# Performance work log

Hardware: AMD Instinct MI355X
Metric: run time of the kernel (lower is better)

The kernel has to match this reference:

```python
import jax, jax.numpy as jnp
import numpy as np
import math

D_MODEL = 1024
N_HEADS = 16
HEAD_DIM = D_MODEL // N_HEADS  # 64
R = HEAD_DIM // 2              # 32
ROPE_BASE = 10000.0
B, T = 4, 2048


def setup_inputs() -> dict:
    key = jax.random.key(0)
    k1, k2, k3, k4, k5 = jax.random.split(key, 5)
    x = jax.random.normal(k1, (B, T, D_MODEL), dtype=jnp.float32)
    Wqkv = jax.random.normal(k2, (3 * D_MODEL, D_MODEL), dtype=jnp.float32) * (1.0 / math.sqrt(D_MODEL))
    Wout = jax.random.normal(k3, (D_MODEL, D_MODEL), dtype=jnp.float32) * (1.0 / math.sqrt(D_MODEL))
    alpha = jax.random.normal(k4, (N_HEADS, R), dtype=jnp.float32) * 0.01
    beta = jax.random.normal(k5, (N_HEADS, R), dtype=jnp.float32) * 0.01
    return {"x": x, "Wqkv": Wqkv, "Wout": Wout, "alpha": alpha, "beta": beta}


def _fourier_bias(alpha, beta, t):
    # omega[r] = base^{-2r/head_dim}, same geometric spacing as RoPE
    omega = ROPE_BASE ** (-2.0 * jnp.arange(R, dtype=jnp.float32) / HEAD_DIM)
    # bias depends only on displacement i-j in [-(t-1), t-1]: compute once per
    # displacement, then gather into the (t, t) matrix (same math as full T x T).
    disp = jnp.arange(-(t - 1), t, dtype=jnp.float32)            # (2t-1,)
    angles = omega[:, None] * disp[None, :]                       # (R, 2t-1)
    vec = jnp.einsum('hr,rk->hk', alpha, jnp.cos(angles)) \
        + jnp.einsum('hr,rk->hk', beta, jnp.sin(angles))          # (H, 2t-1)
    i = jnp.arange(t)
    idx = i[:, None] - i[None, :] + (t - 1)                       # (t, t), delta[i,j]=i-j
    return vec[:, idx]                                            # (H, t, t)


def reference(x, Wqkv, Wout, alpha, beta):
    b, t, d = x.shape
    qkv = x @ Wqkv.T                                              # (B, T, 3D)
    q, k, v = jnp.split(qkv, 3, axis=-1)
    def heads(a):
        return a.reshape(b, t, N_HEADS, HEAD_DIM).transpose(0, 2, 1, 3)  # (B,H,T,dh)
    q, k, v = heads(q), heads(k), heads(v)
    scale = 1.0 / math.sqrt(HEAD_DIM)
    logits = jnp.einsum('bhqd,bhkd->bhqk', q, k) * scale          # (B,H,T,T)
    logits = logits + _fourier_bias(alpha, beta, t)[None]
    causal = jnp.tril(jnp.ones((t, t), dtype=bool))
    logits = jnp.where(causal[None, None], logits, -jnp.inf)
    attn = jax.nn.softmax(logits, axis=-1)
    out = jnp.einsum('bhqk,bhkd->bhqd', attn, v)                  # (B,H,T,dh)
    out = out.transpose(0, 2, 1, 3).reshape(b, t, d)
    return out @ Wout.T
```

## Files before the change

### kernel.cpp

```cpp
#include <hip/hip_runtime.h>
#include <cstdint>
#include <cstddef>

typedef _Float16 f16;
typedef f16 f16x8 __attribute__((ext_vector_type(8)));
typedef __fp16 fp16x2 __attribute__((ext_vector_type(2)));
typedef float f32x4 __attribute__((ext_vector_type(4)));
typedef float f32x16 __attribute__((ext_vector_type(16)));
typedef uint32_t u32;


__device__ __forceinline__ void gload16(const void* g, void* l) {
  __builtin_amdgcn_global_load_lds((const __attribute__((address_space(1))) void*)g,
                                   (__attribute__((address_space(3))) void*)l,
                                   16u, 0, 0u);
}

__device__ __forceinline__ u32 pkrtz(float a, float b) {
  union { fp16x2 v; u32 u; } t;
  t.v = __builtin_amdgcn_cvt_pkrtz(a, b);
  return t.u;
}

__device__ __forceinline__ u32 packh2(float a, float b) { return pkrtz(a, b); }

__device__ __forceinline__ float max3f(float a, float b, float c) {
  return fmaxf(fmaxf(a, b), c);
}

__device__ __forceinline__ void pl32swap(u32& a, u32& b) {
  asm volatile("v_permlane32_swap_b32 %0, %1" : "+v"(a), "+v"(b));
}


__global__ __launch_bounds__(256) void cvt_f32_f16(const float* __restrict__ in,
                                                   f16* __restrict__ out, int n) {
  int i = (blockIdx.x * 256 + threadIdx.x) * 8;
  if (i >= n) return;
  float4 a = *(const float4*)(in + i);
  float4 b = *(const float4*)(in + i + 4);
  f16x8 o;
  o[0] = (f16)a.x; o[1] = (f16)a.y; o[2] = (f16)a.z; o[3] = (f16)a.w;
  o[4] = (f16)b.x; o[5] = (f16)b.y; o[6] = (f16)b.z; o[7] = (f16)b.w;
  *(f16x8*)(out + i) = o;
}


__global__ __launch_bounds__(256) void build_tables(const float* __restrict__ alpha,
                                                    const float* __restrict__ beta,
                                                    f16* __restrict__ U,
                                                    f16* __restrict__ Wt) {
  int idx = blockIdx.x * 256 + threadIdx.x;
  int t = idx >> 5, r = idx & 31;
  float w = powf(10000.0f, -(float)r / 32.0f);
  float ang = w * (float)t;
  float c = cosf(ang), s = sinf(ang);
  const float L2E = 1.44269504089f;
  U[t * 64 + 2 * r]     = (f16)(c * L2E);
  U[t * 64 + 2 * r + 1] = (f16)(s * L2E);
  #pragma unroll
  for (int h = 0; h < 16; ++h) {
    float al = alpha[h * 32 + r], be = beta[h * 32 + r];
    Wt[(size_t)(h * 2048 + t) * 64 + 2 * r]     = (f16)(al * c - be * s);
    Wt[(size_t)(h * 2048 + t) * 64 + 2 * r + 1] = (f16)(al * s + be * c);
  }
}



__global__ __launch_bounds__(512, 2) void gemm_qkv(const f16* __restrict__ A,
                                                   const f16* __restrict__ B,
                                                   f16* __restrict__ Q,
                                                   f16* __restrict__ Kh,
                                                   f16* __restrict__ Vt) {
  __shared__ __align__(16) char sm[147456];
  const int K = 1024;
  int tid = threadIdx.x;
  int lane = tid & 63, wid = tid >> 6;
  int bid = blockIdx.x;
  int xcd = bid & 7;
  int id = bid >> 3;
  int ml = id / 24;
  int nn = id % 24;
  int m0 = (xcd * 4 + ml) * 256;
  int n0 = nn * 128;
  int wm = wid >> 1, wn = wid & 1;
  int c = lane & 15, g = lane >> 4;
  int swz = (c & 7) << 4;

  const f16* asrc[4]; int adst[4];
  #pragma unroll
  for (int i = 0; i < 4; ++i) {
    int p = i * 8192 + tid * 16;
    int row = p >> 7;
    int col = (p & 127) ^ ((row & 7) << 4);
    asrc[i] = A + (size_t)(m0 + row) * K + (col >> 1);
    adst[i] = i * 8192 + wid * 1024;
  }
  const f16* bsrc[2]; int bdst[2];
  #pragma unroll
  for (int i = 0; i < 2; ++i) {
    int p = i * 8192 + tid * 16;
    int row = p >> 7;
    int col = (p & 127) ^ ((row & 7) << 4);
    bsrc[i] = B + (size_t)(n0 + row) * K + (col >> 1);
    bdst[i] = i * 8192 + wid * 1024;
  }

  f32x4 acc[4][4] = {};

  #pragma unroll
  for (int i = 0; i < 4; ++i) gload16(asrc[i], sm + adst[i]);
  #pragma unroll
  for (int i = 0; i < 2; ++i) gload16(bsrc[i], sm + 98304 + bdst[i]);
  #pragma unroll
  for (int i = 0; i < 4; ++i) gload16(asrc[i] + 64, sm + 32768 + adst[i]);
  #pragma unroll
  for (int i = 0; i < 2; ++i) gload16(bsrc[i] + 64, sm + 98304 + 16384 + bdst[i]);

  for (int kt = 0; kt < 16; ++kt) {
    if (kt < 15) asm volatile("s_waitcnt vmcnt(6)" ::: "memory");
    else         asm volatile("s_waitcnt vmcnt(0)" ::: "memory");
    __builtin_amdgcn_s_barrier();

    int j = kt % 3;
    char* As = sm + j * 32768;
    char* Bs = sm + 98304 + j * 16384;
    int jn = (kt + 2) % 3;
    char* Ad = sm + jn * 32768;
    char* Bd = sm + 98304 + jn * 16384;
    bool stg = (kt <= 13);

    if (stg) {
      gload16(asrc[0] + (kt + 2) * 64, Ad + adst[0]);
      gload16(asrc[1] + (kt + 2) * 64, Ad + adst[1]);
      gload16(asrc[2] + (kt + 2) * 64, Ad + adst[2]);
    }
    {
      int co = (g * 16) ^ swz;
      f16x8 af[4], bf[4];
      #pragma unroll
      for (int fr = 0; fr < 4; ++fr)
        af[fr] = *(const f16x8*)(As + (wm * 64 + fr * 16 + c) * 128 + co);
      #pragma unroll
      for (int fn = 0; fn < 4; ++fn)
        bf[fn] = *(const f16x8*)(Bs + (wn * 64 + fn * 16 + c) * 128 + co);
      __builtin_amdgcn_s_setprio(1);
      #pragma unroll
      for (int fr = 0; fr < 4; ++fr)
        #pragma unroll
        for (int fn = 0; fn < 4; ++fn)
          acc[fr][fn] = __builtin_amdgcn_mfma_f32_16x16x32_f16(af[fr], bf[fn], acc[fr][fn], 0, 0, 0);
      __builtin_amdgcn_s_setprio(0);
    }
    if (stg) {
      gload16(asrc[3] + (kt + 2) * 64, Ad + adst[3]);
      gload16(bsrc[0] + (kt + 2) * 64, Bd + bdst[0]);
      gload16(bsrc[1] + (kt + 2) * 64, Bd + bdst[1]);
    }
    {
      int co = (64 + g * 16) ^ swz;
      f16x8 af[4], bf[4];
      #pragma unroll
      for (int fr = 0; fr < 4; ++fr)
        af[fr] = *(const f16x8*)(As + (wm * 64 + fr * 16 + c) * 128 + co);
      #pragma unroll
      for (int fn = 0; fn < 4; ++fn)
        bf[fn] = *(const f16x8*)(Bs + (wn * 64 + fn * 16 + c) * 128 + co);
      __builtin_amdgcn_s_setprio(1);
      #pragma unroll
      for (int fr = 0; fr < 4; ++fr)
        #pragma unroll
        for (int fn = 0; fn < 4; ++fn)
          acc[fr][fn] = __builtin_amdgcn_mfma_f32_16x16x32_f16(af[fr], bf[fn], acc[fr][fn], 0, 0, 0);
      __builtin_amdgcn_s_setprio(0);
    }
  }

  int which = n0 >> 10;
  #pragma unroll
  for (int fr = 0; fr < 4; ++fr) {
    int m = m0 + wm * 64 + fr * 16 + g * 4;
    int b = m >> 11, t = m & 2047;
    #pragma unroll
    for (int fn = 0; fn < 4; ++fn) {
      int n = n0 + wn * 64 + fn * 16 + c;
      int nf = n & 1023, hh = nf >> 6, d = nf & 63;
      if (which == 0) {
        #pragma unroll
        for (int r = 0; r < 4; ++r)
          Q[(size_t)((b * 16 + hh) * 2048 + (t + r)) * 64 + d] = (f16)(acc[fr][fn][r] * 0.180336880111f);
      } else if (which == 1) {
        #pragma unroll
        for (int r = 0; r < 4; ++r)
          Kh[(size_t)((b * 16 + hh) * 2048 + (t + r)) * 64 + d] = (f16)acc[fr][fn][r];
      } else {
        uint2 pk;
        pk.x = packh2(acc[fr][fn][0], acc[fr][fn][1]);
        pk.y = packh2(acc[fr][fn][2], acc[fr][fn][3]);
        *(uint2*)(Vt + (size_t)((b * 16 + hh) * 64 + d) * 2048 + t) = pk;
      }
    }
  }
}


__global__ __launch_bounds__(512, 2) void gemm_out(const f16* __restrict__ A,
                                                   const f16* __restrict__ B,
                                                   float* __restrict__ Cout) {
  __shared__ __align__(16) char sm[147456];
  const int K = 1024;
  int tid = threadIdx.x;
  int lane = tid & 63, wid = tid >> 6;
  int bid = blockIdx.x;
  int xcd = bid & 7;
  int id = bid >> 3;
  int m0 = (xcd * 4 + id / 8) * 256;
  int n0 = (id & 7) * 128;
  int wm = wid >> 1, wn = wid & 1;
  int c = lane & 15, g = lane >> 4;
  int swz = (c & 7) << 4;

  const f16* asrc[4]; int adst[4];
  #pragma unroll
  for (int i = 0; i < 4; ++i) {
    int p = i * 8192 + tid * 16;
    int row = p >> 7;
    int col = (p & 127) ^ ((row & 7) << 4);
    asrc[i] = A + (size_t)(m0 + row) * K + (col >> 1);
    adst[i] = i * 8192 + wid * 1024;
  }
  const f16* bsrc[2]; int bdst[2];
  #pragma unroll
  for (int i = 0; i < 2; ++i) {
    int p = i * 8192 + tid * 16;
    int row = p >> 7;
    int col = (p & 127) ^ ((row & 7) << 4);
    bsrc[i] = B + (size_t)(n0 + row) * K + (col >> 1);
    bdst[i] = i * 8192 + wid * 1024;
  }

  f32x4 acc[4][4] = {};

  #pragma unroll
  for (int i = 0; i < 4; ++i) gload16(asrc[i], sm + adst[i]);
  #pragma unroll
  for (int i = 0; i < 2; ++i) gload16(bsrc[i], sm + 98304 + bdst[i]);
  #pragma unroll
  for (int i = 0; i < 4; ++i) gload16(asrc[i] + 64, sm + 32768 + adst[i]);
  #pragma unroll
  for (int i = 0; i < 2; ++i) gload16(bsrc[i] + 64, sm + 98304 + 16384 + bdst[i]);

  for (int kt = 0; kt < 16; ++kt) {
    if (kt < 15) asm volatile("s_waitcnt vmcnt(6)" ::: "memory");
    else         asm volatile("s_waitcnt vmcnt(0)" ::: "memory");
    __builtin_amdgcn_s_barrier();

    int j = kt % 3;
    char* As = sm + j * 32768;
    char* Bs = sm + 98304 + j * 16384;
    int jn = (kt + 2) % 3;
    char* Ad = sm + jn * 32768;
    char* Bd = sm + 98304 + jn * 16384;
    bool stg = (kt <= 13);

    if (stg) {
      gload16(asrc[0] + (kt + 2) * 64, Ad + adst[0]);
      gload16(asrc[1] + (kt + 2) * 64, Ad + adst[1]);
      gload16(asrc[2] + (kt + 2) * 64, Ad + adst[2]);
    }
    {
      int co = (g * 16) ^ swz;
      f16x8 af[4], bf[4];
      #pragma unroll
      for (int fr = 0; fr < 4; ++fr)
        af[fr] = *(const f16x8*)(As + (wm * 64 + fr * 16 + c) * 128 + co);
      #pragma unroll
      for (int fn = 0; fn < 4; ++fn)
        bf[fn] = *(const f16x8*)(Bs + (wn * 64 + fn * 16 + c) * 128 + co);
      __builtin_amdgcn_s_setprio(1);
      #pragma unroll
      for (int fr = 0; fr < 4; ++fr)
        #pragma unroll
        for (int fn = 0; fn < 4; ++fn)
          acc[fr][fn] = __builtin_amdgcn_mfma_f32_16x16x32_f16(af[fr], bf[fn], acc[fr][fn], 0, 0, 0);
      __builtin_amdgcn_s_setprio(0);
    }
    if (stg) {
      gload16(asrc[3] + (kt + 2) * 64, Ad + adst[3]);
      gload16(bsrc[0] + (kt + 2) * 64, Bd + bdst[0]);
      gload16(bsrc[1] + (kt + 2) * 64, Bd + bdst[1]);
    }
    {
      int co = (64 + g * 16) ^ swz;
      f16x8 af[4], bf[4];
      #pragma unroll
      for (int fr = 0; fr < 4; ++fr)
        af[fr] = *(const f16x8*)(As + (wm * 64 + fr * 16 + c) * 128 + co);
      #pragma unroll
      for (int fn = 0; fn < 4; ++fn)
        bf[fn] = *(const f16x8*)(Bs + (wn * 64 + fn * 16 + c) * 128 + co);
      __builtin_amdgcn_s_setprio(1);
      #pragma unroll
      for (int fr = 0; fr < 4; ++fr)
        #pragma unroll
        for (int fn = 0; fn < 4; ++fn)
          acc[fr][fn] = __builtin_amdgcn_mfma_f32_16x16x32_f16(af[fr], bf[fn], acc[fr][fn], 0, 0, 0);
      __builtin_amdgcn_s_setprio(0);
    }
  }

  #pragma unroll
  for (int fr = 0; fr < 4; ++fr) {
    int m = m0 + wm * 64 + fr * 16 + g * 4;
    #pragma unroll
    for (int fn = 0; fn < 4; ++fn) {
      int n = n0 + wn * 64 + fn * 16 + c;
      #pragma unroll
      for (int r = 0; r < 4; ++r)
        Cout[(size_t)(m + r) * 1024 + n] = acc[fr][fn][r];
    }
  }
}


__global__ __launch_bounds__(512, 2) void attn(const f16* __restrict__ Q,
                                               const f16* __restrict__ Kh,
                                               const f16* __restrict__ Vt,
                                               const f16* __restrict__ U,
                                               const f16* __restrict__ Wt,
                                               f16* __restrict__ AO) {
  __shared__ __align__(16) char sm[98304];
  int tid = threadIdx.x, lane = tid & 63, wid = tid >> 6;
  int l31 = lane & 31, hi = lane >> 5;
  int o = blockIdx.x;
  int pr = o >> 6;
  int bh = o & 63;
  int h = bh & 15, b = bh >> 4;
  int swz = (lane & 15) << 4;

  const f16* ksrc[4]; int kdst[4];
  #pragma unroll
  for (int i = 0; i < 4; ++i) {
    int p = i * 8192 + tid * 16;
    int row = p >> 8;
    int col = (p & 255) ^ ((row & 15) << 4);
    int ce = col >> 1;
    ksrc[i] = (ce < 64) ? (Kh + (size_t)(bh * 2048 + row) * 64 + ce)
                        : (Wt + (size_t)(h * 2048 + row) * 64 + (ce - 64));
    kdst[i] = i * 8192 + wid * 1024;
  }
  const f16* vsrc[2]; int vdst[2];
  #pragma unroll
  for (int i = 0; i < 2; ++i) {
    int p = i * 8192 + tid * 16;
    int row = p >> 8;
    int col = (p & 255) ^ ((row & 15) << 4);
    int ce = col >> 1;
    vsrc[i] = Vt + (size_t)(bh * 64 + row) * 2048 + ce;
    vdst[i] = i * 8192 + wid * 1024;
  }

  #pragma unroll 1
  for (int pass = 0; pass < 2; ++pass) {
    int qt = pass ? pr : 7 - pr;
    int qrow = qt * 256 + wid * 32 + l31;
    int ktmax = 2 * qt + 1;

    f16x8 qf[8];
    {
      const f16* qp = Q + (size_t)(bh * 2048 + qrow) * 64 + hi * 8;
      const f16* up = U + (size_t)qrow * 64 + hi * 8;
      #pragma unroll
      for (int ks = 0; ks < 4; ++ks) {
        qf[ks]     = *(const f16x8*)(qp + ks * 16);
        qf[4 + ks] = *(const f16x8*)(up + ks * 16);
      }
    }

    float m_i = -1e30f, l_i = 0.0f;
    f32x16 accA = {}, accB = {};

    #pragma unroll
    for (int i = 0; i < 4; ++i) gload16(ksrc[i], sm + kdst[i]);
    #pragma unroll
    for (int i = 0; i < 2; ++i) gload16(vsrc[i], sm + 65536 + vdst[i]);
    __syncthreads();

    for (int kt = 0; kt <= ktmax; ++kt) {
      int cur = kt & 1;
      char* Ks = sm + cur * 32768;
      char* Vs = sm + 65536 + cur * 16384;

      if (kt < ktmax) {
        char* kb = sm + (cur ^ 1) * 32768;
        char* vb = sm + 65536 + (cur ^ 1) * 16384;
        #pragma unroll
        for (int i = 0; i < 4; ++i) gload16(ksrc[i] + (size_t)(kt + 1) * 8192, kb + kdst[i]);
        #pragma unroll
        for (int i = 0; i < 2; ++i) gload16(vsrc[i] + (size_t)(kt + 1) * 128, vb + vdst[i]);
      }

      f32x16 st0 = {}, st1 = {}, st2 = {}, st3 = {};
      __builtin_amdgcn_s_setprio(1);
      #pragma unroll
      for (int ks = 0; ks < 8; ++ks) {
        int co = (ks * 32 + hi * 16) ^ swz;
        f16x8 k0 = *(const f16x8*)(Ks + l31 * 256 + co);
        f16x8 k1 = *(const f16x8*)(Ks + (32 + l31) * 256 + co);
        f16x8 k2 = *(const f16x8*)(Ks + (64 + l31) * 256 + co);
        f16x8 k3 = *(const f16x8*)(Ks + (96 + l31) * 256 + co);
        st0 = __builtin_amdgcn_mfma_f32_32x32x16_f16(k0, qf[ks], st0, 0, 0, 0);
        st1 = __builtin_amdgcn_mfma_f32_32x32x16_f16(k1, qf[ks], st1, 0, 0, 0);
        st2 = __builtin_amdgcn_mfma_f32_32x32x16_f16(k2, qf[ks], st2, 0, 0, 0);
        st3 = __builtin_amdgcn_mfma_f32_32x32x16_f16(k3, qf[ks], st3, 0, 0, 0);
      }
      __builtin_amdgcn_s_setprio(0);

      int kv0 = kt * 128;
      if (kv0 + 127 > qt * 256 + wid * 32) {
        #pragma unroll
        for (int r = 0; r < 16; ++r) {
          int kvl = kv0 + (r & 3) + 8 * (r >> 2) + 4 * hi;
          if (kvl > qrow) st0[r] = -1e30f;
          if (kvl + 32 > qrow) st1[r] = -1e30f;
          if (kvl + 64 > qrow) st2[r] = -1e30f;
          if (kvl + 96 > qrow) st3[r] = -1e30f;
        }
      }

      float pm = fmaxf(fmaxf(st0[0], st1[0]), fmaxf(st2[0], st3[0]));
      #pragma unroll
      for (int r = 1; r < 16; ++r) {
        pm = max3f(pm, st0[r], st1[r]);
        pm = max3f(pm, st2[r], st3[r]);
      }
      pm = fmaxf(pm, __shfl_xor(pm, 32, 64));
      if (!__all(pm <= m_i + 8.0f)) {
        float mnew = fmaxf(m_i, pm);
        float sc = __builtin_amdgcn_exp2f(m_i - mnew);
        l_i *= sc;
        accA *= sc;
        accB *= sc;
        m_i = mnew;
      }

      float ps = 0.0f;
      u32 pk0[8], pk1[8], pk2[8], pk3[8];
      #pragma unroll
      for (int j = 0; j < 8; ++j) {
        float a0 = __builtin_amdgcn_exp2f(st0[2 * j] - m_i);
        float a1 = __builtin_amdgcn_exp2f(st0[2 * j + 1] - m_i);
        float b0 = __builtin_amdgcn_exp2f(st1[2 * j] - m_i);
        float b1 = __builtin_amdgcn_exp2f(st1[2 * j + 1] - m_i);
        float c0 = __builtin_amdgcn_exp2f(st2[2 * j] - m_i);
        float c1 = __builtin_amdgcn_exp2f(st2[2 * j + 1] - m_i);
        float d0 = __builtin_amdgcn_exp2f(st3[2 * j] - m_i);
        float d1 = __builtin_amdgcn_exp2f(st3[2 * j + 1] - m_i);
        ps += (a0 + a1) + (b0 + b1) + (c0 + c1) + (d0 + d1);
        pk0[j] = pkrtz(a0, a1);
        pk1[j] = pkrtz(b0, b1);
        pk2[j] = pkrtz(c0, c1);
        pk3[j] = pkrtz(d0, d1);
      }
      ps += __shfl_xor(ps, 32, 64);
      l_i += ps;

      pl32swap(pk0[0], pk0[2]); pl32swap(pk0[1], pk0[3]);
      pl32swap(pk0[4], pk0[6]); pl32swap(pk0[5], pk0[7]);
      pl32swap(pk1[0], pk1[2]); pl32swap(pk1[1], pk1[3]);
      pl32swap(pk1[4], pk1[6]); pl32swap(pk1[5], pk1[7]);
      pl32swap(pk2[0], pk2[2]); pl32swap(pk2[1], pk2[3]);
      pl32swap(pk2[4], pk2[6]); pl32swap(pk2[5], pk2[7]);
      pl32swap(pk3[0], pk3[2]); pl32swap(pk3[1], pk3[3]);
      pl32swap(pk3[4], pk3[6]); pl32swap(pk3[5], pk3[7]);

      __builtin_amdgcn_s_setprio(1);
      #pragma unroll
      for (int kb = 0; kb < 8; ++kb) {
        union { u32 w[4]; f16x8 v; } bf;
        const u32* pk = (kb < 2) ? pk0 : (kb < 4) ? pk1 : (kb < 6) ? pk2 : pk3;
        int base = (kb & 1) * 4;
        bf.w[0] = pk[base + 0]; bf.w[1] = pk[base + 1];
        bf.w[2] = pk[base + 2]; bf.w[3] = pk[base + 3];
        int co = (kb * 32 + hi * 16) ^ swz;
        f16x8 v0 = *(const f16x8*)(Vs + l31 * 256 + co);
        f16x8 v1 = *(const f16x8*)(Vs + (32 + l31) * 256 + co);
        accA = __builtin_amdgcn_mfma_f32_32x32x16_f16(v0, bf.v, accA, 0, 0, 0);
        accB = __builtin_amdgcn_mfma_f32_32x32x16_f16(v1, bf.v, accB, 0, 0, 0);
      }
      __builtin_amdgcn_s_setprio(0);
      __syncthreads();
    }

    float inv = __builtin_amdgcn_rcpf(l_i);
    f16* aop = AO + (size_t)(b * 2048 + qrow) * 1024 + h * 64;
    #pragma unroll
    for (int u = 0; u < 4; ++u) {
      uint2 ov;
      ov.x = pkrtz(accA[4 * u] * inv, accA[4 * u + 1] * inv);
      ov.y = pkrtz(accA[4 * u + 2] * inv, accA[4 * u + 3] * inv);
      *(uint2*)(aop + 8 * u + 4 * hi) = ov;
      ov.x = pkrtz(accB[4 * u] * inv, accB[4 * u + 1] * inv);
      ov.y = pkrtz(accB[4 * u + 2] * inv, accB[4 * u + 3] * inv);
      *(uint2*)(aop + 32 + 8 * u + 4 * hi) = ov;
    }
  }
}


extern "C" void kernel_launch(void* const* d_in, const int* in_sizes, int n_in,
                              void* d_out, int out_size, void* d_ws, size_t ws_size,
                              hipStream_t stream) {
  const float* x     = (const float*)d_in[0];
  const float* Wqkv  = (const float*)d_in[1];
  const float* Wout  = (const float*)d_in[2];
  const float* alpha = (const float*)d_in[3];
  const float* beta  = (const float*)d_in[4];

  char* ws = (char*)d_ws;
  f16* Xh    = (f16*)(ws);
  f16* Wqkvh = (f16*)(ws + 16777216);
  f16* Wouth = (f16*)(ws + 23068672);
  f16* Qh    = (f16*)(ws + 25165824);
  f16* Kh    = (f16*)(ws + 41943040);
  f16* Vt    = (f16*)(ws + 58720256);
  f16* U     = (f16*)(ws + 75497472);
  f16* Wt    = (f16*)(ws + 75759616);
  f16* AO    = Xh;

  cvt_f32_f16<<<4096, 256, 0, stream>>>(x, Xh, 8388608);
  cvt_f32_f16<<<1536, 256, 0, stream>>>(Wqkv, Wqkvh, 3145728);
  cvt_f32_f16<<<512, 256, 0, stream>>>(Wout, Wouth, 1048576);
  build_tables<<<256, 256, 0, stream>>>(alpha, beta, U, Wt);
  gemm_qkv<<<768, 512, 0, stream>>>(Xh, Wqkvh, Qh, Kh, Vt);
  attn<<<256, 512, 0, stream>>>(Qh, Kh, Vt, U, Wt, AO);
  gemm_out<<<256, 512, 0, stream>>>(AO, Wouth, (float*)d_out);
}
```

Measured before the change: 165.1 us.

## Apply Fourier bias as multiplicative exp factor instead of extra QK dimensions

```diff
diff --git a/kernel.cpp b/kernel.cpp
--- a/kernel.cpp
+++ b/kernel.cpp
@@ -23,6 +23,13 @@
 }
 
 __device__ __forceinline__ u32 packh2(float a, float b) { return pkrtz(a, b); }
+
+__device__ __forceinline__ u32 pkmul(u32 a, u32 b) {
+  union { fp16x2 v; u32 u; } x, y, r;
+  x.u = a; y.u = b;
+  r.v = x.v * y.v;
+  return r.u;
+}
 
 __device__ __forceinline__ float max3f(float a, float b, float c) {
   return fmaxf(fmaxf(a, b), c);
@@ -46,26 +53,41 @@
 }
 
 
-__global__ __launch_bounds__(256) void build_tables(const float* __restrict__ alpha,
-                                                    const float* __restrict__ beta,
-                                                    f16* __restrict__ U,
-                                                    f16* __restrict__ Wt) {
+__global__ __launch_bounds__(256) void build_bias(const float* __restrict__ alpha,
+                                                  const float* __restrict__ beta,
+                                                  float* __restrict__ Bias) {
+  int d = blockIdx.x * 256 + threadIdx.x;
+  if (d >= 4095) return;
+  float delta = (float)(d - 2047);
+  float acc[16];
+  #pragma unroll
+  for (int h = 0; h < 16; ++h) acc[h] = 0.0f;
+  for (int r = 0; r < 32; ++r) {
+    float w = powf(10000.0f, -(float)r / 32.0f);
+    float ang = w * delta;
+    float c = cosf(ang), s = sinf(ang);
+    #pragma unroll
+    for (int h = 0; h < 16; ++h)
+      acc[h] += alpha[h * 32 + r] * c + beta[h * 32 + r] * s;
+  }
+  #pragma unroll
+  for (int h = 0; h < 16; ++h) Bias[h * 4095 + d] = acc[h];
+}
+
+__global__ __launch_bounds__(256) void pack_F(const float* __restrict__ Bias,
+                                              uint2* __restrict__ Fdup) {
   int idx = blockIdx.x * 256 + threadIdx.x;
-  int t = idx >> 5, r = idx & 31;
-  float w = powf(10000.0f, -(float)r / 32.0f);
-  float ang = w * (float)t;
-  float c = cosf(ang), s = sinf(ang);
-  const float L2E = 1.44269504089f;
-  U[t * 64 + 2 * r]     = (f16)(c * L2E);
-  U[t * 64 + 2 * r + 1] = (f16)(s * L2E);
-  #pragma unroll
-  for (int h = 0; h < 16; ++h) {
-    float al = alpha[h * 32 + r], be = beta[h * 32 + r];
-    Wt[(size_t)(h * 2048 + t) * 64 + 2 * r]     = (f16)(al * c - be * s);
-    Wt[(size_t)(h * 2048 + t) * 64 + 2 * r + 1] = (f16)(al * s + be * c);
-  }
-}
-
+  if (idx >= 16 * 4095) return;
+  int h = idx / 4095, d = idx - h * 4095;
+  const float* Bh = Bias + h * 4095;
+  int d1 = d - 1 < 0 ? 0 : d - 1;
+  int d2 = d - 2 < 0 ? 0 : d - 2;
+  int d3 = d - 3 < 0 ? 0 : d - 3;
+  uint2 o;
+  o.x = pkrtz(expf(Bh[d]),  expf(Bh[d1]));
+  o.y = pkrtz(expf(Bh[d2]), expf(Bh[d3]));
+  Fdup[idx] = o;
+}
 
 
 __global__ __launch_bounds__(512, 2) void gemm_qkv(const f16* __restrict__ A,
@@ -327,27 +349,27 @@
 __global__ __launch_bounds__(512, 2) void attn(const f16* __restrict__ Q,
                                                const f16* __restrict__ Kh,
                                                const f16* __restrict__ Vt,
-                                               const f16* __restrict__ U,
-                                               const f16* __restrict__ Wt,
+                                               const uint2* __restrict__ Fdup,
                                                f16* __restrict__ AO) {
-  __shared__ __align__(16) char sm[98304];
+  __shared__ __align__(16) char sm[65536];
   int tid = threadIdx.x, lane = tid & 63, wid = tid >> 6;
   int l31 = lane & 31, hi = lane >> 5;
   int o = blockIdx.x;
   int pr = o >> 6;
   int bh = o & 63;
   int h = bh & 15, b = bh >> 4;
-  int swz = (lane & 15) << 4;
-
-  const f16* ksrc[4]; int kdst[4];
-  #pragma unroll
-  for (int i = 0; i < 4; ++i) {
+  int swzK = (lane & 7) << 4;
+  int swzV = (lane & 15) << 4;
+
+  const uint2* Fp = Fdup + (size_t)h * 4095;
+
+  const f16* ksrc[2]; int kdst[2];
+  #pragma unroll
+  for (int i = 0; i < 2; ++i) {
     int p = i * 8192 + tid * 16;
-    int row = p >> 8;
-    int col = (p & 255) ^ ((row & 15) << 4);
-    int ce = col >> 1;
-    ksrc[i] = (ce < 64) ? (Kh + (size_t)(bh * 2048 + row) * 64 + ce)
-                        : (Wt + (size_t)(h * 2048 + row) * 64 + (ce - 64));
+    int row = p >> 7;
+    int col = (p & 127) ^ ((row & 7) << 4);
+    ksrc[i] = Kh + (size_t)(bh * 2048 + row) * 64 + (col >> 1);
     kdst[i] = i * 8192 + wid * 1024;
   }
   const f16* vsrc[2]; int vdst[2];
@@ -356,8 +378,7 @@
     int p = i * 8192 + tid * 16;
     int row = p >> 8;
     int col = (p & 255) ^ ((row & 15) << 4);
-    int ce = col >> 1;
-    vsrc[i] = Vt + (size_t)(bh * 64 + row) * 2048 + ce;
+    vsrc[i] = Vt + (size_t)(bh * 64 + row) * 2048 + (col >> 1);
     vdst[i] = i * 8192 + wid * 1024;
   }
 
@@ -367,49 +388,55 @@
     int qrow = qt * 256 + wid * 32 + l31;
     int ktmax = 2 * qt + 1;
 
-    f16x8 qf[8];
+    f16x8 qf[4];
     {
       const f16* qp = Q + (size_t)(bh * 2048 + qrow) * 64 + hi * 8;
-      const f16* up = U + (size_t)qrow * 64 + hi * 8;
-      #pragma unroll
-      for (int ks = 0; ks < 4; ++ks) {
-        qf[ks]     = *(const f16x8*)(qp + ks * 16);
-        qf[4 + ks] = *(const f16x8*)(up + ks * 16);
-      }
+      #pragma unroll
+      for (int ks = 0; ks < 4; ++ks) qf[ks] = *(const f16x8*)(qp + ks * 16);
     }
 
     float m_i = -1e30f, l_i = 0.0f;
     f32x16 accA = {}, accB = {};
 
     #pragma unroll
-    for (int i = 0; i < 4; ++i) gload16(ksrc[i], sm + kdst[i]);
+    for (int i = 0; i < 2; ++i) gload16(ksrc[i], sm + kdst[i]);
     #pragma unroll
-    for (int i = 0; i < 2; ++i) gload16(vsrc[i], sm + 65536 + vdst[i]);
+    for (int i = 0; i < 2; ++i) gload16(vsrc[i], sm + 32768 + vdst[i]);
     __syncthreads();
 
     for (int kt = 0; kt <= ktmax; ++kt) {
       int cur = kt & 1;
-      char* Ks = sm + cur * 32768;
-      char* Vs = sm + 65536 + cur * 16384;
+      char* Ks = sm + cur * 16384;
+      char* Vs = sm + 32768 + cur * 16384;
 
       if (kt < ktmax) {
-        char* kb = sm + (cur ^ 1) * 32768;
-        char* vb = sm + 65536 + (cur ^ 1) * 16384;
-        #pragma unroll
-        for (int i = 0; i < 4; ++i) gload16(ksrc[i] + (size_t)(kt + 1) * 8192, kb + kdst[i]);
+        char* kb = sm + (cur ^ 1) * 16384;
+        char* vb = sm + 32768 + (cur ^ 1) * 16384;
+        #pragma unroll
+        for (int i = 0; i < 2; ++i) gload16(ksrc[i] + (size_t)(kt + 1) * 8192, kb + kdst[i]);
         #pragma unroll
         for (int i = 0; i < 2; ++i) gload16(vsrc[i] + (size_t)(kt + 1) * 128, vb + vdst[i]);
+      }
+
+      int fidx = qrow - kt * 128 - 4 * hi + 2047;
+      uint2 fw0[4], fw1[4], fw2[4], fw3[4];
+      #pragma unroll
+      for (int rg = 0; rg < 4; ++rg) {
+        fw0[rg] = Fp[fidx - rg * 8];
+        fw1[rg] = Fp[fidx - 32 - rg * 8];
+        fw2[rg] = Fp[fidx - 64 - rg * 8];
+        fw3[rg] = Fp[fidx - 96 - rg * 8];
       }
 
       f32x16 st0 = {}, st1 = {}, st2 = {}, st3 = {};
       __builtin_amdgcn_s_setprio(1);
       #pragma unroll
-      for (int ks = 0; ks < 8; ++ks) {
-        int co = (ks * 32 + hi * 16) ^ swz;
-        f16x8 k0 = *(const f16x8*)(Ks + l31 * 256 + co);
-        f16x8 k1 = *(const f16x8*)(Ks + (32 + l31) * 256 + co);
-        f16x8 k2 = *(const f16x8*)(Ks + (64 + l31) * 256 + co);
-        f16x8 k3 = *(const f16x8*)(Ks + (96 + l31) * 256 + co);
+      for (int ks = 0; ks < 4; ++ks) {
+        int co = (ks * 32 + hi * 16) ^ swzK;
+        f16x8 k0 = *(const f16x8*)(Ks + l31 * 128 + co);
+        f16x8 k1 = *(const f16x8*)(Ks + (32 + l31) * 128 + co);
+        f16x8 k2 = *(const f16x8*)(Ks + (64 + l31) * 128 + co);
+        f16x8 k3 = *(const f16x8*)(Ks + (96 + l31) * 128 + co);
         st0 = __builtin_amdgcn_mfma_f32_32x32x16_f16(k0, qf[ks], st0, 0, 0, 0);
         st1 = __builtin_amdgcn_mfma_f32_32x32x16_f16(k1, qf[ks], st1, 0, 0, 0);
         st2 = __builtin_amdgcn_mfma_f32_32x32x16_f16(k2, qf[ks], st2, 0, 0, 0);
@@ -449,6 +476,11 @@
       u32 pk0[8], pk1[8], pk2[8], pk3[8];
       #pragma unroll
       for (int j = 0; j < 8; ++j) {
+        int rg = j >> 1;
+        u32 w0 = (j & 1) ? fw0[rg].y : fw0[rg].x;
+        u32 w1 = (j & 1) ? fw1[rg].y : fw1[rg].x;
+        u32 w2 = (j & 1) ? fw2[rg].y : fw2[rg].x;
+        u32 w3 = (j & 1) ? fw3[rg].y : fw3[rg].x;
         float a0 = __builtin_amdgcn_exp2f(st0[2 * j] - m_i);
         float a1 = __builtin_amdgcn_exp2f(st0[2 * j + 1] - m_i);
         float b0 = __builtin_amdgcn_exp2f(st1[2 * j] - m_i);
@@ -457,11 +489,14 @@
         float c1 = __builtin_amdgcn_exp2f(st2[2 * j + 1] - m_i);
         float d0 = __builtin_amdgcn_exp2f(st3[2 * j] - m_i);
         float d1 = __builtin_amdgcn_exp2f(st3[2 * j + 1] - m_i);
-        ps += (a0 + a1) + (b0 + b1) + (c0 + c1) + (d0 + d1);
-        pk0[j] = pkrtz(a0, a1);
-        pk1[j] = pkrtz(b0, b1);
-        pk2[j] = pkrtz(c0, c1);
-        pk3[j] = pkrtz(d0, d1);
+        pk0[j] = pkmul(pkrtz(a0, a1), w0);
+        pk1[j] = pkmul(pkrtz(b0, b1), w1);
+        pk2[j] = pkmul(pkrtz(c0, c1), w2);
+        pk3[j] = pkmul(pkrtz(d0, d1), w3);
+        union { fp16x2 v; u32 u; } s0, s1, s2, s3;
+        s0.u = pk0[j]; s1.u = pk1[j]; s2.u = pk2[j]; s3.u = pk3[j];
+        ps += (float)s0.v[0] + (float)s0.v[1] + (float)s1.v[0] + (float)s1.v[1];
+        ps += (float)s2.v[0] + (float)s2.v[1] + (float)s3.v[0] + (float)s3.v[1];
       }
       ps += __shfl_xor(ps, 32, 64);
       l_i += ps;
@@ -483,7 +518,7 @@
         int base = (kb & 1) * 4;
         bf.w[0] = pk[base + 0]; bf.w[1] = pk[base + 1];
         bf.w[2] = pk[base + 2]; bf.w[3] = pk[base + 3];
-        int co = (kb * 32 + hi * 16) ^ swz;
+        int co = (kb * 32 + hi * 16) ^ swzV;
         f16x8 v0 = *(const f16x8*)(Vs + l31 * 256 + co);
         f16x8 v1 = *(const f16x8*)(Vs + (32 + l31) * 256 + co);
         accA = __builtin_amdgcn_mfma_f32_32x32x16_f16(v0, bf.v, accA, 0, 0, 0);
@@ -519,21 +554,22 @@
   const float* beta  = (const float*)d_in[4];
 
   char* ws = (char*)d_ws;
-  f16* Xh    = (f16*)(ws);
-  f16* Wqkvh = (f16*)(ws + 16777216);
-  f16* Wouth = (f16*)(ws + 23068672);
-  f16* Qh    = (f16*)(ws + 25165824);
-  f16* Kh    = (f16*)(ws + 41943040);
-  f16* Vt    = (f16*)(ws + 58720256);
-  f16* U     = (f16*)(ws + 75497472);
-  f16* Wt    = (f16*)(ws + 75759616);
-  f16* AO    = Xh;
+  f16* Xh      = (f16*)(ws);
+  f16* Wqkvh   = (f16*)(ws + 16777216);
+  f16* Wouth   = (f16*)(ws + 23068672);
+  f16* Qh      = (f16*)(ws + 25165824);
+  f16* Kh      = (f16*)(ws + 41943040);
+  f16* Vt      = (f16*)(ws + 58720256);
+  float* BiasT = (float*)(ws + 75497472);
+  uint2* Fdup  = (uint2*)(ws + 75759616);
+  f16* AO      = Xh;
 
   cvt_f32_f16<<<4096, 256, 0, stream>>>(x, Xh, 8388608);
   cvt_f32_f16<<<1536, 256, 0, stream>>>(Wqkv, Wqkvh, 3145728);
   cvt_f32_f16<<<512, 256, 0, stream>>>(Wout, Wouth, 1048576);
-  build_tables<<<256, 256, 0, stream>>>(alpha, beta, U, Wt);
+  build_bias<<<16, 256, 0, stream>>>(alpha, beta, BiasT);
+  pack_F<<<256, 256, 0, stream>>>(BiasT, Fdup);
   gemm_qkv<<<768, 512, 0, stream>>>(Xh, Wqkvh, Qh, Kh, Vt);
-  attn<<<256, 512, 0, stream>>>(Qh, Kh, Vt, U, Wt, AO);
+  attn<<<256, 512, 0, stream>>>(Qh, Kh, Vt, Fdup, AO);
   gemm_out<<<256, 512, 0, stream>>>(AO, Wouth, (float*)d_out);
 }
```

Result: slower. 189.4 us (+14.7%).

## Halve attention block tiles to 128 queries and 64-key steps with 4 waves

Applied to the files above, without the earlier changes.

```diff
diff --git a/kernel.cpp b/kernel.cpp
--- a/kernel.cpp
+++ b/kernel.cpp
@@ -65,7 +65,6 @@
     Wt[(size_t)(h * 2048 + t) * 64 + 2 * r + 1] = (f16)(al * s + be * c);
   }
 }
-
 
 
 __global__ __launch_bounds__(512, 2) void gemm_qkv(const f16* __restrict__ A,
@@ -324,47 +323,47 @@
 }
 
 
-__global__ __launch_bounds__(512, 2) void attn(const f16* __restrict__ Q,
+__global__ __launch_bounds__(256, 2) void attn(const f16* __restrict__ Q,
                                                const f16* __restrict__ Kh,
                                                const f16* __restrict__ Vt,
                                                const f16* __restrict__ U,
                                                const f16* __restrict__ Wt,
                                                f16* __restrict__ AO) {
-  __shared__ __align__(16) char sm[98304];
+  __shared__ __align__(16) char sm[49152];
   int tid = threadIdx.x, lane = tid & 63, wid = tid >> 6;
   int l31 = lane & 31, hi = lane >> 5;
   int o = blockIdx.x;
   int pr = o >> 6;
   int bh = o & 63;
   int h = bh & 15, b = bh >> 4;
-  int swz = (lane & 15) << 4;
+  int swzK = (lane & 15) << 4;
+  int swzV = (lane & 7) << 4;
 
   const f16* ksrc[4]; int kdst[4];
   #pragma unroll
   for (int i = 0; i < 4; ++i) {
-    int p = i * 8192 + tid * 16;
+    int p = i * 4096 + tid * 16;
     int row = p >> 8;
     int col = (p & 255) ^ ((row & 15) << 4);
     int ce = col >> 1;
     ksrc[i] = (ce < 64) ? (Kh + (size_t)(bh * 2048 + row) * 64 + ce)
                         : (Wt + (size_t)(h * 2048 + row) * 64 + (ce - 64));
-    kdst[i] = i * 8192 + wid * 1024;
+    kdst[i] = i * 4096 + wid * 1024;
   }
   const f16* vsrc[2]; int vdst[2];
   #pragma unroll
   for (int i = 0; i < 2; ++i) {
-    int p = i * 8192 + tid * 16;
-    int row = p >> 8;
-    int col = (p & 255) ^ ((row & 15) << 4);
-    int ce = col >> 1;
-    vsrc[i] = Vt + (size_t)(bh * 64 + row) * 2048 + ce;
-    vdst[i] = i * 8192 + wid * 1024;
+    int p = i * 4096 + tid * 16;
+    int row = p >> 7;
+    int col = (p & 127) ^ ((row & 7) << 4);
+    vsrc[i] = Vt + (size_t)(bh * 64 + row) * 2048 + (col >> 1);
+    vdst[i] = i * 4096 + wid * 1024;
   }
 
   #pragma unroll 1
   for (int pass = 0; pass < 2; ++pass) {
-    int qt = pass ? pr : 7 - pr;
-    int qrow = qt * 256 + wid * 32 + l31;
+    int qt = pass ? pr : 15 - pr;
+    int qrow = qt * 128 + wid * 32 + l31;
     int ktmax = 2 * qt + 1;
 
     f16x8 qf[8];
@@ -384,57 +383,48 @@
     #pragma unroll
     for (int i = 0; i < 4; ++i) gload16(ksrc[i], sm + kdst[i]);
     #pragma unroll
-    for (int i = 0; i < 2; ++i) gload16(vsrc[i], sm + 65536 + vdst[i]);
+    for (int i = 0; i < 2; ++i) gload16(vsrc[i], sm + 32768 + vdst[i]);
     __syncthreads();
 
     for (int kt = 0; kt <= ktmax; ++kt) {
       int cur = kt & 1;
-      char* Ks = sm + cur * 32768;
-      char* Vs = sm + 65536 + cur * 16384;
+      char* Ks = sm + cur * 16384;
+      char* Vs = sm + 32768 + cur * 8192;
 
       if (kt < ktmax) {
-        char* kb = sm + (cur ^ 1) * 32768;
-        char* vb = sm + 65536 + (cur ^ 1) * 16384;
-        #pragma unroll
-        for (int i = 0; i < 4; ++i) gload16(ksrc[i] + (size_t)(kt + 1) * 8192, kb + kdst[i]);
-        #pragma unroll
-        for (int i = 0; i < 2; ++i) gload16(vsrc[i] + (size_t)(kt + 1) * 128, vb + vdst[i]);
-      }
-
-      f32x16 st0 = {}, st1 = {}, st2 = {}, st3 = {};
+        char* kb = sm + (cur ^ 1) * 16384;
+        char* vb = sm + 32768 + (cur ^ 1) * 8192;
+        #pragma unroll
+        for (int i = 0; i < 4; ++i) gload16(ksrc[i] + (size_t)(kt + 1) * 4096, kb + kdst[i]);
+        #pragma unroll
+        for (int i = 0; i < 2; ++i) gload16(vsrc[i] + (size_t)(kt + 1) * 64, vb + vdst[i]);
+      }
+
+      f32x16 st0 = {}, st1 = {};
       __builtin_amdgcn_s_setprio(1);
       #pragma unroll
       for (int ks = 0; ks < 8; ++ks) {
-        int co = (ks * 32 + hi * 16) ^ swz;
+        int co = (ks * 32 + hi * 16) ^ swzK;
         f16x8 k0 = *(const f16x8*)(Ks + l31 * 256 + co);
         f16x8 k1 = *(const f16x8*)(Ks + (32 + l31) * 256 + co);
-        f16x8 k2 = *(const f16x8*)(Ks + (64 + l31) * 256 + co);
-        f16x8 k3 = *(const f16x8*)(Ks + (96 + l31) * 256 + co);
         st0 = __builtin_amdgcn_mfma_f32_32x32x16_f16(k0, qf[ks], st0, 0, 0, 0);
         st1 = __builtin_amdgcn_mfma_f32_32x32x16_f16(k1, qf[ks], st1, 0, 0, 0);
-        st2 = __builtin_amdgcn_mfma_f32_32x32x16_f16(k2, qf[ks], st2, 0, 0, 0);
-        st3 = __builtin_amdgcn_mfma_f32_32x32x16_f16(k3, qf[ks], st3, 0, 0, 0);
       }
       __builtin_amdgcn_s_setprio(0);
 
-      int kv0 = kt * 128;
-      if (kv0 + 127 > qt * 256 + wid * 32) {
+      int kv0 = kt * 64;
+      if (kv0 + 63 > qt * 128 + wid * 32) {
         #pragma unroll
         for (int r = 0; r < 16; ++r) {
           int kvl = kv0 + (r & 3) + 8 * (r >> 2) + 4 * hi;
           if (kvl > qrow) st0[r] = -1e30f;
           if (kvl + 32 > qrow) st1[r] = -1e30f;
-          if (kvl + 64 > qrow) st2[r] = -1e30f;
-          if (kvl + 96 > qrow) st3[r] = -1e30f;
         }
       }
 
-      float pm = fmaxf(fmaxf(st0[0], st1[0]), fmaxf(st2[0], st3[0]));
-      #pragma unroll
-      for (int r = 1; r < 16; ++r) {
-        pm = max3f(pm, st0[r], st1[r]);
-        pm = max3f(pm, st2[r], st3[r]);
-      }
+      float pm = fmaxf(st0[0], st1[0]);
+      #pragma unroll
+      for (int r = 1; r < 16; ++r) pm = max3f(pm, st0[r], st1[r]);
       pm = fmaxf(pm, __shfl_xor(pm, 32, 64));
       if (!__all(pm <= m_i + 8.0f)) {
         float mnew = fmaxf(m_i, pm);
@@ -446,22 +436,16 @@
       }
 
       float ps = 0.0f;
-      u32 pk0[8], pk1[8], pk2[8], pk3[8];
+      u32 pk0[8], pk1[8];
       #pragma unroll
       for (int j = 0; j < 8; ++j) {
         float a0 = __builtin_amdgcn_exp2f(st0[2 * j] - m_i);
         float a1 = __builtin_amdgcn_exp2f(st0[2 * j + 1] - m_i);
         float b0 = __builtin_amdgcn_exp2f(st1[2 * j] - m_i);
         float b1 = __builtin_amdgcn_exp2f(st1[2 * j + 1] - m_i);
-        float c0 = __builtin_amdgcn_exp2f(st2[2 * j] - m_i);
-        float c1 = __builtin_amdgcn_exp2f(st2[2 * j + 1] - m_i);
-        float d0 = __builtin_amdgcn_exp2f(st3[2 * j] - m_i);
-        float d1 = __builtin_amdgcn_exp2f(st3[2 * j + 1] - m_i);
-        ps += (a0 + a1) + (b0 + b1) + (c0 + c1) + (d0 + d1);
+        ps += (a0 + a1) + (b0 + b1);
         pk0[j] = pkrtz(a0, a1);
         pk1[j] = pkrtz(b0, b1);
-        pk2[j] = pkrtz(c0, c1);
-        pk3[j] = pkrtz(d0, d1);
       }
       ps += __shfl_xor(ps, 32, 64);
       l_i += ps;
@@ -470,22 +454,18 @@
       pl32swap(pk0[4], pk0[6]); pl32swap(pk0[5], pk0[7]);
       pl32swap(pk1[0], pk1[2]); pl32swap(pk1[1], pk1[3]);
       pl32swap(pk1[4], pk1[6]); pl32swap(pk1[5], pk1[7]);
-      pl32swap(pk2[0], pk2[2]); pl32swap(pk2[1], pk2[3]);
-      pl32swap(pk2[4], pk2[6]); pl32swap(pk2[5], pk2[7]);
-      pl32swap(pk3[0], pk3[2]); pl32swap(pk3[1], pk3[3]);
-      pl32swap(pk3[4], pk3[6]); pl32swap(pk3[5], pk3[7]);
 
       __builtin_amdgcn_s_setprio(1);
       #pragma unroll
-      for (int kb = 0; kb < 8; ++kb) {
+      for (int kb = 0; kb < 4; ++kb) {
         union { u32 w[4]; f16x8 v; } bf;
-        const u32* pk = (kb < 2) ? pk0 : (kb < 4) ? pk1 : (kb < 6) ? pk2 : pk3;
+        const u32* pk = (kb < 2) ? pk0 : pk1;
         int base = (kb & 1) * 4;
         bf.w[0] = pk[base + 0]; bf.w[1] = pk[base + 1];
         bf.w[2] = pk[base + 2]; bf.w[3] = pk[base + 3];
-        int co = (kb * 32 + hi * 16) ^ swz;
-        f16x8 v0 = *(const f16x8*)(Vs + l31 * 256 + co);
-        f16x8 v1 = *(const f16x8*)(Vs + (32 + l31) * 256 + co);
+        int co = (kb * 32 + hi * 16) ^ swzV;
+        f16x8 v0 = *(const f16x8*)(Vs + l31 * 128 + co);
+        f16x8 v1 = *(const f16x8*)(Vs + (32 + l31) * 128 + co);
         accA = __builtin_amdgcn_mfma_f32_32x32x16_f16(v0, bf.v, accA, 0, 0, 0);
         accB = __builtin_amdgcn_mfma_f32_32x32x16_f16(v1, bf.v, accB, 0, 0, 0);
       }
@@ -534,6 +514,6 @@
   cvt_f32_f16<<<512, 256, 0, stream>>>(Wout, Wouth, 1048576);
   build_tables<<<256, 256, 0, stream>>>(alpha, beta, U, Wt);
   gemm_qkv<<<768, 512, 0, stream>>>(Xh, Wqkvh, Qh, Kh, Vt);
-  attn<<<256, 512, 0, stream>>>(Qh, Kh, Vt, U, Wt, AO);
+  attn<<<512, 256, 0, stream>>>(Qh, Kh, Vt, U, Wt, AO);
   gemm_out<<<256, 512, 0, stream>>>(AO, Wouth, (float*)d_out);
 }
```

After: 166.3 us. No clear change (+0.7%).
